# Optimization experiments

Hardware: AMD Instinct MI355X
Metric: run time of the kernel (lower is better)

Reference implementation:

```python
import jax, jax.numpy as jnp
import numpy as np

NUM_C = 1024
EMB = 512
HID = 512
BATCH = 64
SEQ = 512


def setup_inputs() -> dict:
    key = jax.random.key(0)
    ks = jax.random.split(key, 10)
    q = jax.random.randint(ks[0], (BATCH, SEQ), 0, NUM_C, dtype=jnp.int32)
    r = jax.random.randint(ks[1], (BATCH, SEQ), 0, 2, dtype=jnp.int32)
    s = 1.0 / np.sqrt(HID)
    emb = jax.random.normal(ks[2], (NUM_C * 2, EMB), dtype=jnp.float32)
    Wh_w = jax.random.uniform(ks[3], (HID, HID), jnp.float32, -s, s)
    Wh_b = jax.random.uniform(ks[4], (HID,), jnp.float32, -s, s)
    Wx_w = jax.random.uniform(ks[5], (HID, EMB), jnp.float32, -s, s)
    Wx_b = jax.random.uniform(ks[6], (HID,), jnp.float32, -s, s)
    tau = jnp.ones((HID,), jnp.float32)
    Wo_w = jax.random.uniform(ks[7], (NUM_C, HID), jnp.float32, -s, s)
    Wo_b = jax.random.uniform(ks[8], (NUM_C,), jnp.float32, -s, s)
    return {"q": q, "r": r, "emb": emb, "Wh_w": Wh_w, "Wh_b": Wh_b,
            "Wx_w": Wx_w, "Wx_b": Wx_b, "tau": tau, "Wo_w": Wo_w, "Wo_b": Wo_b}


def reference(q, r, emb, Wh_w, Wh_b, Wx_w, Wx_b, tau, Wo_w, Wo_b):
    # interaction embedding: x = q + num_c * r
    idx = q + NUM_C * r                      # [B, S]
    xemb = emb[idx]                          # [B, S, E]
    # precompute input projection for all timesteps (faithful: same sum)
    xproj = jnp.einsum('bse,he->bsh', xemb, Wx_w) + Wx_b + Wh_b  # [B, S, H]

    def step(h, xp_t):
        # liquid time-constant cell update
        dh = (-h + jnp.tanh(h @ Wh_w.T + xp_t)) / tau
        h_new = h + dh
        return h_new, h_new

    h0 = jnp.zeros((q.shape[0], HID), xemb.dtype)
    _, hs = jax.lax.scan(step, h0, jnp.swapaxes(xproj, 0, 1))  # hs: [S, B, H]
    outputs = jnp.swapaxes(hs, 0, 1)         # [B, S, H]
    # dropout is identity at inference
    y = jax.nn.sigmoid(jnp.einsum('bsh,ch->bsc', outputs, Wo_w) + Wo_b)
    return y
```

## Files before the change

### kernel.cpp

```cpp
#include <hip/hip_runtime.h>
#include <hip/hip_bf16.h>

#define NUM_C 1024
#define EMB   512
#define HID   512
#define BATCH 64
#define SEQ   512

typedef short bf16x8 __attribute__((ext_vector_type(8)));
typedef float f32x4  __attribute__((ext_vector_type(4)));

__device__ __forceinline__ unsigned short f2bf(float x) {
    unsigned u = __float_as_uint(x);
    u += 0x7fffu + ((u >> 16) & 1u);
    return (unsigned short)(u >> 16);
}
__device__ __forceinline__ float uaf(unsigned u) { return __uint_as_float(u); }

__device__ __forceinline__ float ftanh(float x) {
    float e = __expf(2.f * x);
    return 1.f - 2.f / (e + 1.f);
}

__global__ __launch_bounds__(256) void f32_to_bf16(const float* __restrict__ src,
                                                   unsigned short* __restrict__ dst, int n) {
    int i = blockIdx.x * 256 + threadIdx.x;
    if (i < n) dst[i] = f2bf(src[i]);
}

__global__ __launch_bounds__(256)
void gemm_nt_f32(const float* __restrict__ A, const float* __restrict__ B,
                 float* __restrict__ C, int M, int N, int K,
                 const float* __restrict__ bias1, const float* __restrict__ bias2) {
    __shared__ float As[64][33];
    __shared__ float Bs[64][33];

    const int n0 = blockIdx.x * 64;
    const int m0 = blockIdx.y * 64;
    const int tid = threadIdx.x;
    const int tx = tid & 15;
    const int ty = tid >> 4;

    float acc[4][4] = {{0.f}};

    for (int k0 = 0; k0 < K; k0 += 32) {
        #pragma unroll
        for (int i = 0; i < 2; ++i) {
            int f   = tid * 2 + i;
            int row = f >> 3;
            int kf  = f & 7;
            float4 va = *(const float4*)&A[(size_t)(m0 + row) * K + k0 + kf * 4];
            float4 vb = *(const float4*)&B[(size_t)(n0 + row) * K + k0 + kf * 4];
            As[row][kf * 4 + 0] = va.x; As[row][kf * 4 + 1] = va.y;
            As[row][kf * 4 + 2] = va.z; As[row][kf * 4 + 3] = va.w;
            Bs[row][kf * 4 + 0] = vb.x; Bs[row][kf * 4 + 1] = vb.y;
            Bs[row][kf * 4 + 2] = vb.z; Bs[row][kf * 4 + 3] = vb.w;
        }
        __syncthreads();
        #pragma unroll
        for (int kk = 0; kk < 32; ++kk) {
            float a[4], b[4];
            #pragma unroll
            for (int i = 0; i < 4; ++i) a[i] = As[ty * 4 + i][kk];
            #pragma unroll
            for (int j = 0; j < 4; ++j) b[j] = Bs[tx * 4 + j][kk];
            #pragma unroll
            for (int i = 0; i < 4; ++i)
                #pragma unroll
                for (int j = 0; j < 4; ++j)
                    acc[i][j] += a[i] * b[j];
        }
        __syncthreads();
    }

    float bb[4];
    #pragma unroll
    for (int j = 0; j < 4; ++j) {
        int n = n0 + tx * 4 + j;
        bb[j] = bias1[n] + bias2[n];
    }
    #pragma unroll
    for (int i = 0; i < 4; ++i) {
        size_t m = (size_t)(m0 + ty * 4 + i);
        float4 ov;
        ov.x = acc[i][0] + bb[0]; ov.y = acc[i][1] + bb[1];
        ov.z = acc[i][2] + bb[2]; ov.w = acc[i][3] + bb[3];
        *(float4*)&C[m * N + n0 + tx * 4] = ov;
    }
}

__global__ __launch_bounds__(512, 2)
void ltc_scan5(const int* __restrict__ q, const int* __restrict__ r,
               const float* __restrict__ emb_proj, const float* __restrict__ Wh,
               const float* __restrict__ tau, unsigned short* __restrict__ hs_bf) {
    __shared__ float hfA[512], hfB[512], psA[512], psB[512];
    __shared__ int idA[512], idB[512];

    const int tid  = threadIdx.x;
    const int sl   = blockIdx.x >> 5;
    const int bp   = blockIdx.x & 31;
    const int bA   = bp * 2, bB = bA + 1;
    const int lane = tid & 63;
    const int w    = tid >> 6;

    float4 wr_[16];
    {
        const float* wrow = Wh + (size_t)(sl * 64 + lane) * 512 + w * 64;
        #pragma unroll
        for (int i = 0; i < 16; ++i) wr_[i] = ((const float4*)wrow)[i];
    }

    hfA[tid] = 0.f; hfB[tid] = 0.f;
    idA[tid] = q[bA * SEQ + tid] + NUM_C * r[bA * SEQ + tid];
    idB[tid] = q[bB * SEQ + tid] + NUM_C * r[bB * SEQ + tid];

    const bool fin = (w == sl);
    float rtau = 0.f, hA = 0.f, hB = 0.f, embA = 0.f, embB = 0.f;
    if (fin) rtau = 1.0f / tau[sl * 64 + lane];

    unsigned* hswA = (unsigned*)(hs_bf + (size_t)bA * SEQ * HID);
    unsigned* hswB = (unsigned*)(hs_bf + (size_t)bB * SEQ * HID);
    __syncthreads();

    if (fin) {
        embA = emb_proj[(size_t)idA[0] * HID + sl * 64 + lane];
        embB = emb_proj[(size_t)idB[0] * HID + sl * 64 + lane];
    }

    for (int s = 0; s < SEQ; ++s) {
        if (fin) {
            if (s > 0) {
                float pre = embB;
                #pragma unroll
                for (int m = 0; m < 8; ++m) pre += psB[m * 64 + lane];
                float hn = hB + (ftanh(pre) - hB) * rtau;
                hB = hn;
                hfB[sl * 64 + lane] = hn;
                unsigned us = f2bf(hn);
                unsigned ot = (unsigned)__shfl_xor((int)us, 1);
                if (!(lane & 1))
                    __hip_atomic_store(&hswB[(s - 1) * 256 + sl * 32 + (lane >> 1)],
                                       us | (ot << 16), __ATOMIC_RELAXED,
                                       __HIP_MEMORY_SCOPE_AGENT);
                embB = emb_proj[(size_t)idB[s] * HID + sl * 64 + lane];
            }
        } else if (s > 0 && lane < 32) {
            unsigned* ap = &hswA[(s - 1) * 256 + w * 32 + lane];
            unsigned word = __hip_atomic_load(ap, __ATOMIC_RELAXED, __HIP_MEMORY_SCOPE_AGENT);
            while ((word & 0xffffu) == 0x7f7fu) {
                __builtin_amdgcn_s_sleep(1);
                word = __hip_atomic_load(ap, __ATOMIC_RELAXED, __HIP_MEMORY_SCOPE_AGENT);
            }
            float2 hv; hv.x = uaf(word << 16); hv.y = uaf(word & 0xffff0000u);
            *(float2*)&hfA[w * 64 + 2 * lane] = hv;
        }
        {
            const float4* hv4 = (const float4*)(hfA + w * 64);
            float a0 = 0.f, a1 = 0.f, a2 = 0.f, a3 = 0.f;
            #pragma unroll
            for (int i = 0; i < 16; ++i) {
                float4 hv = hv4[i];
                a0 += wr_[i].x * hv.x; a1 += wr_[i].y * hv.y;
                a2 += wr_[i].z * hv.z; a3 += wr_[i].w * hv.w;
            }
            psA[w * 64 + lane] = (a0 + a1) + (a2 + a3);
        }
        __syncthreads();

        if (fin) {
            float pre = embA;
            #pragma unroll
            for (int m = 0; m < 8; ++m) pre += psA[m * 64 + lane];
            float hn = hA + (ftanh(pre) - hA) * rtau;
            hA = hn;
            hfA[sl * 64 + lane] = hn;
            unsigned us = f2bf(hn);
            unsigned ot = (unsigned)__shfl_xor((int)us, 1);
            if (!(lane & 1))
                __hip_atomic_store(&hswA[s * 256 + sl * 32 + (lane >> 1)],
                                   us | (ot << 16), __ATOMIC_RELAXED,
                                   __HIP_MEMORY_SCOPE_AGENT);
            if (s + 1 < SEQ)
                embA = emb_proj[(size_t)idA[s + 1] * HID + sl * 64 + lane];
        } else if (s > 0 && lane < 32) {
            unsigned* ap = &hswB[(s - 1) * 256 + w * 32 + lane];
            unsigned word = __hip_atomic_load(ap, __ATOMIC_RELAXED, __HIP_MEMORY_SCOPE_AGENT);
            while ((word & 0xffffu) == 0x7f7fu) {
                __builtin_amdgcn_s_sleep(1);
                word = __hip_atomic_load(ap, __ATOMIC_RELAXED, __HIP_MEMORY_SCOPE_AGENT);
            }
            float2 hv; hv.x = uaf(word << 16); hv.y = uaf(word & 0xffff0000u);
            *(float2*)&hfB[w * 64 + 2 * lane] = hv;
        }
        {
            const float4* hv4 = (const float4*)(hfB + w * 64);
            float a0 = 0.f, a1 = 0.f, a2 = 0.f, a3 = 0.f;
            #pragma unroll
            for (int i = 0; i < 16; ++i) {
                float4 hv = hv4[i];
                a0 += wr_[i].x * hv.x; a1 += wr_[i].y * hv.y;
                a2 += wr_[i].z * hv.z; a3 += wr_[i].w * hv.w;
            }
            psB[w * 64 + lane] = (a0 + a1) + (a2 + a3);
        }
        __syncthreads();
    }

    if (fin) {
        float pre = embB;
        #pragma unroll
        for (int m = 0; m < 8; ++m) pre += psB[m * 64 + lane];
        float hn = hB + (ftanh(pre) - hB) * rtau;
        unsigned us = f2bf(hn);
        unsigned ot = (unsigned)__shfl_xor((int)us, 1);
        if (!(lane & 1))
            __hip_atomic_store(&hswB[(SEQ - 1) * 256 + sl * 32 + (lane >> 1)],
                               us | (ot << 16), __ATOMIC_RELAXED,
                               __HIP_MEMORY_SCOPE_AGENT);
    }
}

__global__ __launch_bounds__(256)
void gemm_out_bf16(const unsigned short* __restrict__ A,
                   const unsigned short* __restrict__ B,
                   const float* __restrict__ bias,
                   float* __restrict__ C, int M) {
    __shared__ __align__(16) unsigned short As[128 * 32];
    __shared__ __align__(16) unsigned short Bs[128 * 32];

    const int tid = threadIdx.x;
    const int n0 = blockIdx.x * 128;
    const int m0 = blockIdx.y * 128;
    const int w  = tid >> 6;
    const int l  = tid & 63;
    const int wr = w >> 1, wc = w & 1;
    const int lr = l & 15;
    const int lq = l >> 4;

    f32x4 acc[4][4];
    #pragma unroll
    for (int i = 0; i < 4; ++i)
        #pragma unroll
        for (int jn = 0; jn < 4; ++jn)
            acc[i][jn] = (f32x4){0.f, 0.f, 0.f, 0.f};

    for (int k0 = 0; k0 < 512; k0 += 32) {
        #pragma unroll
        for (int p = 0; p < 2; ++p) {
            int flat = p * 256 + tid;
            int row  = flat >> 2;
            int c4   = flat & 3;
            *(uint4*)&As[row * 32 + c4 * 8] =
                *(const uint4*)&A[(size_t)(m0 + row) * 512 + k0 + c4 * 8];
            *(uint4*)&Bs[row * 32 + c4 * 8] =
                *(const uint4*)&B[(size_t)(n0 + row) * 512 + k0 + c4 * 8];
        }
        __syncthreads();

        bf16x8 af[4], bf[4];
        #pragma unroll
        for (int mf = 0; mf < 4; ++mf)
            af[mf] = *(const bf16x8*)&As[(wr * 64 + mf * 16 + lr) * 32 + lq * 8];
        #pragma unroll
        for (int nf = 0; nf < 4; ++nf)
            bf[nf] = *(const bf16x8*)&Bs[(wc * 64 + nf * 16 + lr) * 32 + lq * 8];

        #pragma unroll
        for (int mf = 0; mf < 4; ++mf)
            #pragma unroll
            for (int nf = 0; nf < 4; ++nf)
                acc[mf][nf] = __builtin_amdgcn_mfma_f32_16x16x32_bf16(
                    af[mf], bf[nf], acc[mf][nf], 0, 0, 0);
        __syncthreads();
    }

    #pragma unroll
    for (int mf = 0; mf < 4; ++mf) {
        #pragma unroll
        for (int nf = 0; nf < 4; ++nf) {
            int col = n0 + wc * 64 + nf * 16 + lr;
            float bb = bias[col];
            #pragma unroll
            for (int reg = 0; reg < 4; ++reg) {
                int rowm = m0 + wr * 64 + mf * 16 + lq * 4 + reg;
                float v = acc[mf][nf][reg] + bb;
                C[(size_t)rowm * 1024 + col] = 1.0f / (1.0f + expf(-v));
            }
        }
    }
}

extern "C" void kernel_launch(void* const* d_in, const int* in_sizes, int n_in,
                              void* d_out, int out_size, void* d_ws, size_t ws_size,
                              hipStream_t stream) {
    const int*   q    = (const int*)d_in[0];
    const int*   r    = (const int*)d_in[1];
    const float* emb  = (const float*)d_in[2];
    const float* Wh_w = (const float*)d_in[3];
    const float* Wh_b = (const float*)d_in[4];
    const float* Wx_w = (const float*)d_in[5];
    const float* Wx_b = (const float*)d_in[6];
    const float* tau  = (const float*)d_in[7];
    const float* Wo_w = (const float*)d_in[8];
    const float* Wo_b = (const float*)d_in[9];
    float* out = (float*)d_out;

    char* ws = (char*)d_ws;
    float*          emb_proj = (float*)ws;
    unsigned short* Wobf     = (unsigned short*)(ws + (4u << 20));
    unsigned short* hs_bf    = (unsigned short*)(ws + (5u << 20));

    hipMemsetAsync(hs_bf, 0x7F, (size_t)BATCH * SEQ * HID * 2, stream);

    f32_to_bf16<<<(1024 * 512) / 256, 256, 0, stream>>>(Wo_w, Wobf, 1024 * 512);

    gemm_nt_f32<<<dim3(512 / 64, 2048 / 64), 256, 0, stream>>>(
        emb, Wx_w, emb_proj, 2048, 512, 512, Wx_b, Wh_b);

    ltc_scan5<<<256, 512, 0, stream>>>(q, r, emb_proj, Wh_w, tau, hs_bf);

    gemm_out_bf16<<<dim3(1024 / 128, (BATCH * SEQ) / 128), 256, 0, stream>>>(
        hs_bf, Wobf, Wo_b, out, BATCH * SEQ);
}
```

Measured before the change: 946.0 us.

## Spread LTC finalize across all waves with shuffle reduction

Before, a single wave per block reduced all 8 partial sums for its 64 hidden units and ran the tanh update while the other waves polled. Now every wave finalizes 8 hidden units, using a cross-lane shuffle reduction over the partial sums, so the serial tail between barriers is shorter. The loop is also reordered so each batch's finalize is followed directly by the poll for the other batch's next state, and the h vector is loaded into registers before the FMA loop. In exchange, seven waves now publish to global memory every step and only 8 lanes per wave do useful finalize work.

Result: slower. 1.305 ms (+37.9%).

```diff
diff --git a/kernel.cpp b/kernel.cpp
--- a/kernel.cpp
+++ b/kernel.cpp
@@ -90,7 +90,7 @@
 }
 
 __global__ __launch_bounds__(512, 2)
-void ltc_scan5(const int* __restrict__ q, const int* __restrict__ r,
+void ltc_scan6(const int* __restrict__ q, const int* __restrict__ r,
                const float* __restrict__ emb_proj, const float* __restrict__ Wh,
                const float* __restrict__ tau, unsigned short* __restrict__ hs_bf) {
     __shared__ float hfA[512], hfB[512], psA[512], psB[512];
@@ -114,109 +114,115 @@
     idA[tid] = q[bA * SEQ + tid] + NUM_C * r[bA * SEQ + tid];
     idB[tid] = q[bB * SEQ + tid] + NUM_C * r[bB * SEQ + tid];
 
-    const bool fin = (w == sl);
+    const int frow = sl * 64 + w * 8 + lane;
     float rtau = 0.f, hA = 0.f, hB = 0.f, embA = 0.f, embB = 0.f;
-    if (fin) rtau = 1.0f / tau[sl * 64 + lane];
+    if (lane < 8) rtau = 1.0f / tau[frow];
 
     unsigned* hswA = (unsigned*)(hs_bf + (size_t)bA * SEQ * HID);
     unsigned* hswB = (unsigned*)(hs_bf + (size_t)bB * SEQ * HID);
+    const float4* hA4 = (const float4*)(hfA + w * 64);
+    const float4* hB4 = (const float4*)(hfB + w * 64);
     __syncthreads();
 
-    if (fin) {
-        embA = emb_proj[(size_t)idA[0] * HID + sl * 64 + lane];
-        embB = emb_proj[(size_t)idB[0] * HID + sl * 64 + lane];
+    if (lane < 8) {
+        embA = emb_proj[(size_t)idA[0] * HID + frow];
+        embB = emb_proj[(size_t)idB[0] * HID + frow];
     }
 
     for (int s = 0; s < SEQ; ++s) {
-        if (fin) {
-            if (s > 0) {
-                float pre = embB;
-                #pragma unroll
-                for (int m = 0; m < 8; ++m) pre += psB[m * 64 + lane];
+        {
+            float4 hb[16];
+            #pragma unroll
+            for (int i = 0; i < 16; ++i) hb[i] = hA4[i];
+            float a0 = 0.f, a1 = 0.f, a2 = 0.f, a3 = 0.f;
+            #pragma unroll
+            for (int i = 0; i < 16; ++i) {
+                a0 += wr_[i].x * hb[i].x; a1 += wr_[i].y * hb[i].y;
+                a2 += wr_[i].z * hb[i].z; a3 += wr_[i].w * hb[i].w;
+            }
+            psA[w * 64 + lane] = (a0 + a1) + (a2 + a3);
+        }
+        __syncthreads();
+
+        {
+            float p = psA[(lane >> 3) * 64 + w * 8 + (lane & 7)];
+            p += __shfl_xor(p, 8); p += __shfl_xor(p, 16); p += __shfl_xor(p, 32);
+            unsigned us = 0;
+            if (lane < 8) {
+                float pre = embA + p;
+                float hn = hA + (ftanh(pre) - hA) * rtau;
+                hA = hn;
+                hfA[frow] = hn;
+                us = f2bf(hn);
+            }
+            unsigned ot = (unsigned)__shfl_xor((int)us, 1);
+            if (lane < 8 && !(lane & 1))
+                __hip_atomic_store(&hswA[s * 256 + sl * 32 + w * 4 + (lane >> 1)],
+                                   us | (ot << 16), __ATOMIC_RELAXED,
+                                   __HIP_MEMORY_SCOPE_AGENT);
+            if (lane < 8 && s + 1 < SEQ)
+                embA = emb_proj[(size_t)idA[s + 1] * HID + frow];
+
+            if (w != sl && s > 0 && lane < 32) {
+                unsigned* ap = &hswB[(s - 1) * 256 + w * 32 + lane];
+                unsigned word = __hip_atomic_load(ap, __ATOMIC_RELAXED,
+                                                  __HIP_MEMORY_SCOPE_AGENT);
+                while ((word & 0xffffu) == 0x7f7fu) {
+                    __builtin_amdgcn_s_sleep(1);
+                    word = __hip_atomic_load(ap, __ATOMIC_RELAXED,
+                                             __HIP_MEMORY_SCOPE_AGENT);
+                }
+                float2 hv; hv.x = uaf(word << 16); hv.y = uaf(word & 0xffff0000u);
+                *(float2*)&hfB[w * 64 + 2 * lane] = hv;
+            }
+        }
+
+        {
+            float4 hb[16];
+            #pragma unroll
+            for (int i = 0; i < 16; ++i) hb[i] = hB4[i];
+            float a0 = 0.f, a1 = 0.f, a2 = 0.f, a3 = 0.f;
+            #pragma unroll
+            for (int i = 0; i < 16; ++i) {
+                a0 += wr_[i].x * hb[i].x; a1 += wr_[i].y * hb[i].y;
+                a2 += wr_[i].z * hb[i].z; a3 += wr_[i].w * hb[i].w;
+            }
+            psB[w * 64 + lane] = (a0 + a1) + (a2 + a3);
+        }
+        __syncthreads();
+
+        {
+            float p = psB[(lane >> 3) * 64 + w * 8 + (lane & 7)];
+            p += __shfl_xor(p, 8); p += __shfl_xor(p, 16); p += __shfl_xor(p, 32);
+            unsigned us = 0;
+            if (lane < 8) {
+                float pre = embB + p;
                 float hn = hB + (ftanh(pre) - hB) * rtau;
                 hB = hn;
-                hfB[sl * 64 + lane] = hn;
-                unsigned us = f2bf(hn);
-                unsigned ot = (unsigned)__shfl_xor((int)us, 1);
-                if (!(lane & 1))
-                    __hip_atomic_store(&hswB[(s - 1) * 256 + sl * 32 + (lane >> 1)],
-                                       us | (ot << 16), __ATOMIC_RELAXED,
-                                       __HIP_MEMORY_SCOPE_AGENT);
-                embB = emb_proj[(size_t)idB[s] * HID + sl * 64 + lane];
-            }
-        } else if (s > 0 && lane < 32) {
-            unsigned* ap = &hswA[(s - 1) * 256 + w * 32 + lane];
-            unsigned word = __hip_atomic_load(ap, __ATOMIC_RELAXED, __HIP_MEMORY_SCOPE_AGENT);
-            while ((word & 0xffffu) == 0x7f7fu) {
-                __builtin_amdgcn_s_sleep(1);
-                word = __hip_atomic_load(ap, __ATOMIC_RELAXED, __HIP_MEMORY_SCOPE_AGENT);
-            }
-            float2 hv; hv.x = uaf(word << 16); hv.y = uaf(word & 0xffff0000u);
-            *(float2*)&hfA[w * 64 + 2 * lane] = hv;
-        }
-        {
-            const float4* hv4 = (const float4*)(hfA + w * 64);
-            float a0 = 0.f, a1 = 0.f, a2 = 0.f, a3 = 0.f;
-            #pragma unroll
-            for (int i = 0; i < 16; ++i) {
-                float4 hv = hv4[i];
-                a0 += wr_[i].x * hv.x; a1 += wr_[i].y * hv.y;
-                a2 += wr_[i].z * hv.z; a3 += wr_[i].w * hv.w;
-            }
-            psA[w * 64 + lane] = (a0 + a1) + (a2 + a3);
-        }
-        __syncthreads();
-
-        if (fin) {
-            float pre = embA;
-            #pragma unroll
-            for (int m = 0; m < 8; ++m) pre += psA[m * 64 + lane];
-            float hn = hA + (ftanh(pre) - hA) * rtau;
-            hA = hn;
-            hfA[sl * 64 + lane] = hn;
-            unsigned us = f2bf(hn);
+                hfB[frow] = hn;
+                us = f2bf(hn);
+            }
             unsigned ot = (unsigned)__shfl_xor((int)us, 1);
-            if (!(lane & 1))
-                __hip_atomic_store(&hswA[s * 256 + sl * 32 + (lane >> 1)],
+            if (lane < 8 && !(lane & 1))
+                __hip_atomic_store(&hswB[s * 256 + sl * 32 + w * 4 + (lane >> 1)],
                                    us | (ot << 16), __ATOMIC_RELAXED,
                                    __HIP_MEMORY_SCOPE_AGENT);
-            if (s + 1 < SEQ)
-                embA = emb_proj[(size_t)idA[s + 1] * HID + sl * 64 + lane];
-        } else if (s > 0 && lane < 32) {
-            unsigned* ap = &hswB[(s - 1) * 256 + w * 32 + lane];
-            unsigned word = __hip_atomic_load(ap, __ATOMIC_RELAXED, __HIP_MEMORY_SCOPE_AGENT);
-            while ((word & 0xffffu) == 0x7f7fu) {
-                __builtin_amdgcn_s_sleep(1);
-                word = __hip_atomic_load(ap, __ATOMIC_RELAXED, __HIP_MEMORY_SCOPE_AGENT);
-            }
-            float2 hv; hv.x = uaf(word << 16); hv.y = uaf(word & 0xffff0000u);
-            *(float2*)&hfB[w * 64 + 2 * lane] = hv;
-        }
-        {
-            const float4* hv4 = (const float4*)(hfB + w * 64);
-            float a0 = 0.f, a1 = 0.f, a2 = 0.f, a3 = 0.f;
-            #pragma unroll
-            for (int i = 0; i < 16; ++i) {
-                float4 hv = hv4[i];
-                a0 += wr_[i].x * hv.x; a1 += wr_[i].y * hv.y;
-                a2 += wr_[i].z * hv.z; a3 += wr_[i].w * hv.w;
-            }
-            psB[w * 64 + lane] = (a0 + a1) + (a2 + a3);
-        }
-        __syncthreads();
-    }
-
-    if (fin) {
-        float pre = embB;
-        #pragma unroll
-        for (int m = 0; m < 8; ++m) pre += psB[m * 64 + lane];
-        float hn = hB + (ftanh(pre) - hB) * rtau;
-        unsigned us = f2bf(hn);
-        unsigned ot = (unsigned)__shfl_xor((int)us, 1);
-        if (!(lane & 1))
-            __hip_atomic_store(&hswB[(SEQ - 1) * 256 + sl * 32 + (lane >> 1)],
-                               us | (ot << 16), __ATOMIC_RELAXED,
-                               __HIP_MEMORY_SCOPE_AGENT);
+            if (lane < 8 && s + 1 < SEQ)
+                embB = emb_proj[(size_t)idB[s + 1] * HID + frow];
+
+            if (w != sl && s + 1 < SEQ && lane < 32) {
+                unsigned* ap = &hswA[s * 256 + w * 32 + lane];
+                unsigned word = __hip_atomic_load(ap, __ATOMIC_RELAXED,
+                                                  __HIP_MEMORY_SCOPE_AGENT);
+                while ((word & 0xffffu) == 0x7f7fu) {
+                    __builtin_amdgcn_s_sleep(1);
+                    word = __hip_atomic_load(ap, __ATOMIC_RELAXED,
+                                             __HIP_MEMORY_SCOPE_AGENT);
+                }
+                float2 hv; hv.x = uaf(word << 16); hv.y = uaf(word & 0xffff0000u);
+                *(float2*)&hfA[w * 64 + 2 * lane] = hv;
+            }
+        }
     }
 }
 
@@ -317,7 +323,7 @@
     gemm_nt_f32<<<dim3(512 / 64, 2048 / 64), 256, 0, stream>>>(
         emb, Wx_w, emb_proj, 2048, 512, 512, Wx_b, Wh_b);
 
-    ltc_scan5<<<256, 512, 0, stream>>>(q, r, emb_proj, Wh_w, tau, hs_bf);
+    ltc_scan6<<<256, 512, 0, stream>>>(q, r, emb_proj, Wh_w, tau, hs_bf);
 
     gemm_out_bf16<<<dim3(1024 / 128, (BATCH * SEQ) / 128), 256, 0, stream>>>(
         hs_bf, Wobf, Wo_b, out, BATCH * SEQ);
```

## Exchange fp32 hidden states between scan blocks and convert to bf16 in output GEMM

Applied to the files above, without the earlier changes.

The scan kernel now publishes each hidden value as a full fp32 word (sentinel 0xFFFFFFFF, detected by an all-ones exponent) instead of packed bf16 pairs. This removes the shuffle and packing from the critical path and lets all 64 lanes poll. The A/B interleaving is restructured so the A step is followed by the B update, with explicit FMAs. The output GEMM converts fp32 to bf16 on load, at the cost of twice the memset and hidden-state traffic.

After: 943.2 us. About the same (-0.3%).

```diff
diff --git a/kernel.cpp b/kernel.cpp
--- a/kernel.cpp
+++ b/kernel.cpp
@@ -14,6 +14,9 @@
     unsigned u = __float_as_uint(x);
     u += 0x7fffu + ((u >> 16) & 1u);
     return (unsigned short)(u >> 16);
+}
+__device__ __forceinline__ unsigned pack2bf(float a, float b) {
+    return (unsigned)f2bf(a) | ((unsigned)f2bf(b) << 16);
 }
 __device__ __forceinline__ float uaf(unsigned u) { return __uint_as_float(u); }
 
@@ -90,11 +93,12 @@
 }
 
 __global__ __launch_bounds__(512, 2)
-void ltc_scan5(const int* __restrict__ q, const int* __restrict__ r,
-               const float* __restrict__ emb_proj, const float* __restrict__ Wh,
-               const float* __restrict__ tau, unsigned short* __restrict__ hs_bf) {
-    __shared__ float hfA[512], hfB[512], psA[512], psB[512];
-    __shared__ int idA[512], idB[512];
+void ltc_scan15(const int* __restrict__ q, const int* __restrict__ r,
+                const float* __restrict__ emb_proj, const float* __restrict__ Wh,
+                const float* __restrict__ tau, float* __restrict__ hx) {
+    __shared__ float hfA[512], hfB[512];
+    __shared__ float psA[512], psB[512];
+    __shared__ int   idA[512], idB[512];
 
     const int tid  = threadIdx.x;
     const int sl   = blockIdx.x >> 5;
@@ -111,117 +115,104 @@
     }
 
     hfA[tid] = 0.f; hfB[tid] = 0.f;
+    psA[tid] = 0.f;
     idA[tid] = q[bA * SEQ + tid] + NUM_C * r[bA * SEQ + tid];
     idB[tid] = q[bB * SEQ + tid] + NUM_C * r[bB * SEQ + tid];
 
     const bool fin = (w == sl);
-    float rtau = 0.f, hA = 0.f, hB = 0.f, embA = 0.f, embB = 0.f;
+    float rtau = 0.f, hA = 0.f, hB = 0.f, eA = 0.f, eB = 0.f;
     if (fin) rtau = 1.0f / tau[sl * 64 + lane];
 
-    unsigned* hswA = (unsigned*)(hs_bf + (size_t)bA * SEQ * HID);
-    unsigned* hswB = (unsigned*)(hs_bf + (size_t)bB * SEQ * HID);
+    float* hxA = hx + (size_t)bA * SEQ * HID;
+    float* hxB = hx + (size_t)bB * SEQ * HID;
+    const float4* hA4 = (const float4*)(hfA + w * 64);
+    const float4* hB4 = (const float4*)(hfB + w * 64);
     __syncthreads();
 
     if (fin) {
-        embA = emb_proj[(size_t)idA[0] * HID + sl * 64 + lane];
-        embB = emb_proj[(size_t)idB[0] * HID + sl * 64 + lane];
+        eA = emb_proj[(size_t)idA[0] * HID + sl * 64 + lane];
+        eB = emb_proj[(size_t)idB[0] * HID + sl * 64 + lane];
     }
 
     for (int s = 0; s < SEQ; ++s) {
         if (fin) {
-            if (s > 0) {
-                float pre = embB;
-                #pragma unroll
-                for (int m = 0; m < 8; ++m) pre += psB[m * 64 + lane];
-                float hn = hB + (ftanh(pre) - hB) * rtau;
-                hB = hn;
-                hfB[sl * 64 + lane] = hn;
-                unsigned us = f2bf(hn);
-                unsigned ot = (unsigned)__shfl_xor((int)us, 1);
-                if (!(lane & 1))
-                    __hip_atomic_store(&hswB[(s - 1) * 256 + sl * 32 + (lane >> 1)],
-                                       us | (ot << 16), __ATOMIC_RELAXED,
-                                       __HIP_MEMORY_SCOPE_AGENT);
-                embB = emb_proj[(size_t)idB[s] * HID + sl * 64 + lane];
-            }
-        } else if (s > 0 && lane < 32) {
-            unsigned* ap = &hswA[(s - 1) * 256 + w * 32 + lane];
-            unsigned word = __hip_atomic_load(ap, __ATOMIC_RELAXED, __HIP_MEMORY_SCOPE_AGENT);
-            while ((word & 0xffffu) == 0x7f7fu) {
-                __builtin_amdgcn_s_sleep(1);
-                word = __hip_atomic_load(ap, __ATOMIC_RELAXED, __HIP_MEMORY_SCOPE_AGENT);
-            }
-            float2 hv; hv.x = uaf(word << 16); hv.y = uaf(word & 0xffff0000u);
-            *(float2*)&hfA[w * 64 + 2 * lane] = hv;
-        }
-        {
-            const float4* hv4 = (const float4*)(hfA + w * 64);
-            float a0 = 0.f, a1 = 0.f, a2 = 0.f, a3 = 0.f;
-            #pragma unroll
-            for (int i = 0; i < 16; ++i) {
-                float4 hv = hv4[i];
-                a0 += wr_[i].x * hv.x; a1 += wr_[i].y * hv.y;
-                a2 += wr_[i].z * hv.z; a3 += wr_[i].w * hv.w;
-            }
-            psA[w * 64 + lane] = (a0 + a1) + (a2 + a3);
-        }
-        __syncthreads();
-
-        if (fin) {
-            float pre = embA;
+            float pre = eA;
             #pragma unroll
             for (int m = 0; m < 8; ++m) pre += psA[m * 64 + lane];
             float hn = hA + (ftanh(pre) - hA) * rtau;
             hA = hn;
+            __hip_atomic_store((unsigned*)&hxA[s * 512 + sl * 64 + lane],
+                               __float_as_uint(hn), __ATOMIC_RELAXED,
+                               __HIP_MEMORY_SCOPE_AGENT);
             hfA[sl * 64 + lane] = hn;
-            unsigned us = f2bf(hn);
-            unsigned ot = (unsigned)__shfl_xor((int)us, 1);
-            if (!(lane & 1))
-                __hip_atomic_store(&hswA[s * 256 + sl * 32 + (lane >> 1)],
-                                   us | (ot << 16), __ATOMIC_RELAXED,
-                                   __HIP_MEMORY_SCOPE_AGENT);
             if (s + 1 < SEQ)
-                embA = emb_proj[(size_t)idA[s + 1] * HID + sl * 64 + lane];
-        } else if (s > 0 && lane < 32) {
-            unsigned* ap = &hswB[(s - 1) * 256 + w * 32 + lane];
-            unsigned word = __hip_atomic_load(ap, __ATOMIC_RELAXED, __HIP_MEMORY_SCOPE_AGENT);
-            while ((word & 0xffffu) == 0x7f7fu) {
+                eA = emb_proj[(size_t)idA[s + 1] * HID + sl * 64 + lane];
+        } else if (s > 0) {
+            unsigned* ap = (unsigned*)&hxB[(s - 1) * 512 + w * 64 + lane];
+            unsigned wi = __hip_atomic_load(ap, __ATOMIC_RELAXED,
+                                            __HIP_MEMORY_SCOPE_AGENT);
+            while ((wi & 0x7f800000u) == 0x7f800000u) {
                 __builtin_amdgcn_s_sleep(1);
-                word = __hip_atomic_load(ap, __ATOMIC_RELAXED, __HIP_MEMORY_SCOPE_AGENT);
-            }
-            float2 hv; hv.x = uaf(word << 16); hv.y = uaf(word & 0xffff0000u);
-            *(float2*)&hfB[w * 64 + 2 * lane] = hv;
+                wi = __hip_atomic_load(ap, __ATOMIC_RELAXED,
+                                       __HIP_MEMORY_SCOPE_AGENT);
+            }
+            hfB[w * 64 + lane] = uaf(wi);
         }
         {
-            const float4* hv4 = (const float4*)(hfB + w * 64);
             float a0 = 0.f, a1 = 0.f, a2 = 0.f, a3 = 0.f;
             #pragma unroll
             for (int i = 0; i < 16; ++i) {
-                float4 hv = hv4[i];
-                a0 += wr_[i].x * hv.x; a1 += wr_[i].y * hv.y;
-                a2 += wr_[i].z * hv.z; a3 += wr_[i].w * hv.w;
+                float4 hv = hB4[i];
+                a0 = fmaf(wr_[i].x, hv.x, a0);
+                a1 = fmaf(wr_[i].y, hv.y, a1);
+                a2 = fmaf(wr_[i].z, hv.z, a2);
+                a3 = fmaf(wr_[i].w, hv.w, a3);
             }
             psB[w * 64 + lane] = (a0 + a1) + (a2 + a3);
         }
         __syncthreads();
-    }
-
-    if (fin) {
-        float pre = embB;
-        #pragma unroll
-        for (int m = 0; m < 8; ++m) pre += psB[m * 64 + lane];
-        float hn = hB + (ftanh(pre) - hB) * rtau;
-        unsigned us = f2bf(hn);
-        unsigned ot = (unsigned)__shfl_xor((int)us, 1);
-        if (!(lane & 1))
-            __hip_atomic_store(&hswB[(SEQ - 1) * 256 + sl * 32 + (lane >> 1)],
-                               us | (ot << 16), __ATOMIC_RELAXED,
+
+        if (fin) {
+            float pre = eB;
+            #pragma unroll
+            for (int m = 0; m < 8; ++m) pre += psB[m * 64 + lane];
+            float hn = hB + (ftanh(pre) - hB) * rtau;
+            hB = hn;
+            __hip_atomic_store((unsigned*)&hxB[s * 512 + sl * 64 + lane],
+                               __float_as_uint(hn), __ATOMIC_RELAXED,
                                __HIP_MEMORY_SCOPE_AGENT);
+            hfB[sl * 64 + lane] = hn;
+            if (s + 1 < SEQ)
+                eB = emb_proj[(size_t)idB[s + 1] * HID + sl * 64 + lane];
+        } else if (s + 1 < SEQ) {
+            unsigned* ap = (unsigned*)&hxA[s * 512 + w * 64 + lane];
+            unsigned wi = __hip_atomic_load(ap, __ATOMIC_RELAXED,
+                                            __HIP_MEMORY_SCOPE_AGENT);
+            while ((wi & 0x7f800000u) == 0x7f800000u) {
+                __builtin_amdgcn_s_sleep(1);
+                wi = __hip_atomic_load(ap, __ATOMIC_RELAXED,
+                                       __HIP_MEMORY_SCOPE_AGENT);
+            }
+            hfA[w * 64 + lane] = uaf(wi);
+        }
+        if (s + 1 < SEQ) {
+            float a0 = 0.f, a1 = 0.f, a2 = 0.f, a3 = 0.f;
+            #pragma unroll
+            for (int i = 0; i < 16; ++i) {
+                float4 hv = hA4[i];
+                a0 = fmaf(wr_[i].x, hv.x, a0);
+                a1 = fmaf(wr_[i].y, hv.y, a1);
+                a2 = fmaf(wr_[i].z, hv.z, a2);
+                a3 = fmaf(wr_[i].w, hv.w, a3);
+            }
+            psA[w * 64 + lane] = (a0 + a1) + (a2 + a3);
+        }
+        __syncthreads();
     }
 }
 
 __global__ __launch_bounds__(256)
-void gemm_out_bf16(const unsigned short* __restrict__ A,
+void gemm_out_bf16(const float* __restrict__ A,
                    const unsigned short* __restrict__ B,
                    const float* __restrict__ bias,
                    float* __restrict__ C, int M) {
@@ -250,8 +241,13 @@
             int flat = p * 256 + tid;
             int row  = flat >> 2;
             int c4   = flat & 3;
-            *(uint4*)&As[row * 32 + c4 * 8] =
-                *(const uint4*)&A[(size_t)(m0 + row) * 512 + k0 + c4 * 8];
+            const float* asrc = &A[(size_t)(m0 + row) * 512 + k0 + c4 * 8];
+            float4 v0 = ((const float4*)asrc)[0];
+            float4 v1 = ((const float4*)asrc)[1];
+            uint4 d;
+            d.x = pack2bf(v0.x, v0.y); d.y = pack2bf(v0.z, v0.w);
+            d.z = pack2bf(v1.x, v1.y); d.w = pack2bf(v1.z, v1.w);
+            *(uint4*)&As[row * 32 + c4 * 8] = d;
             *(uint4*)&Bs[row * 32 + c4 * 8] =
                 *(const uint4*)&B[(size_t)(n0 + row) * 512 + k0 + c4 * 8];
         }
@@ -308,17 +304,17 @@
     char* ws = (char*)d_ws;
     float*          emb_proj = (float*)ws;
     unsigned short* Wobf     = (unsigned short*)(ws + (4u << 20));
-    unsigned short* hs_bf    = (unsigned short*)(ws + (5u << 20));
-
-    hipMemsetAsync(hs_bf, 0x7F, (size_t)BATCH * SEQ * HID * 2, stream);
+    float*          hx       = (float*)(ws + (5u << 20));
+
+    hipMemsetAsync(hx, 0xFF, (size_t)BATCH * SEQ * HID * 4, stream);
 
     f32_to_bf16<<<(1024 * 512) / 256, 256, 0, stream>>>(Wo_w, Wobf, 1024 * 512);
 
     gemm_nt_f32<<<dim3(512 / 64, 2048 / 64), 256, 0, stream>>>(
         emb, Wx_w, emb_proj, 2048, 512, 512, Wx_b, Wh_b);
 
-    ltc_scan5<<<256, 512, 0, stream>>>(q, r, emb_proj, Wh_w, tau, hs_bf);
+    ltc_scan15<<<256, 512, 0, stream>>>(q, r, emb_proj, Wh_w, tau, hx);
 
     gemm_out_bf16<<<dim3(1024 / 128, (BATCH * SEQ) / 128), 256, 0, stream>>>(
-        hs_bf, Wobf, Wo_b, out, BATCH * SEQ);
-}
+        hx, Wobf, Wo_b, out, BATCH * SEQ);
+}
```
